# Kernel optimization log

Hardware: AMD Instinct MI355X
Metric: run time of the kernel (lower is better)

Reference implementation:

```python
import jax, jax.numpy as jnp
import numpy as np

N_NODES = 50000
N_EDGES = 800000
N_GRAPHS = 500
DIM = 64          # node feature dim
NG = 64           # num gaussians (edge rbf dim)
CUTOFF = 12.0
NCONV = 3
HID = 128
NTYPES = 100      # atom vocabulary for embedding
EPS = 1e-5        # batchnorm eps


def _bn(x, g, b):
    # training-mode batchnorm over the leading (edge/node) axis
    m = jnp.mean(x, axis=0)
    v = jnp.var(x, axis=0)
    return g * (x - m) * jax.lax.rsqrt(v + EPS) + b


def setup_inputs() -> dict:
    key = jax.random.key(0)
    ks = jax.random.split(key, 12)
    atom_types = jax.random.randint(ks[0], (N_NODES,), 0, NTYPES)
    src = jax.random.randint(ks[1], (N_EDGES,), 0, N_NODES)
    dst = jax.random.randint(ks[2], (N_EDGES,), 0, N_NODES)
    graph_ids = jnp.sort(jax.random.randint(ks[3], (N_NODES,), 0, N_GRAPHS))
    distance = jax.random.uniform(ks[4], (N_EDGES,), dtype=jnp.float32) * CUTOFF
    cin = 2 * DIM + NG
    s = 0.05
    embed_table = jax.random.normal(ks[5], (NTYPES, DIM), dtype=jnp.float32) * s
    W1 = jax.random.normal(ks[6], (NCONV, cin, DIM), dtype=jnp.float32) * s
    b1 = jnp.zeros((NCONV, DIM), jnp.float32)
    W2 = jax.random.normal(ks[7], (NCONV, cin, DIM), dtype=jnp.float32) * s
    b2 = jnp.zeros((NCONV, DIM), jnp.float32)
    g1 = jnp.ones((NCONV, DIM), jnp.float32); bt1 = jnp.zeros((NCONV, DIM), jnp.float32)
    g2 = jnp.ones((NCONV, DIM), jnp.float32); bt2 = jnp.zeros((NCONV, DIM), jnp.float32)
    g3 = jnp.ones((NCONV, DIM), jnp.float32); bt3 = jnp.zeros((NCONV, DIM), jnp.float32)
    Wfc = jax.random.normal(ks[8], (DIM, HID), dtype=jnp.float32) * s
    bfc = jnp.zeros((HID,), jnp.float32)
    Wout = jax.random.normal(ks[9], (HID, 1), dtype=jnp.float32) * s
    bout = jnp.zeros((1,), jnp.float32)
    return dict(atom_types=atom_types, src=src, dst=dst, graph_ids=graph_ids,
                distance=distance, embed_table=embed_table,
                W1=W1, b1=b1, W2=W2, b2=b2,
                g1=g1, bt1=bt1, g2=g2, bt2=bt2, g3=g3, bt3=bt3,
                Wfc=Wfc, bfc=bfc, Wout=Wout, bout=bout)


def reference(atom_types, src, dst, graph_ids, distance, embed_table,
              W1, b1, W2, b2, g1, bt1, g2, bt2, g3, bt3,
              Wfc, bfc, Wout, bout):
    # embedding lookup
    node = embed_table[atom_types]                           # [N, DIM]
    # RBF expansion of distances (gaussian smearing on [0, CUTOFF])
    mu = jnp.linspace(0.0, CUTOFF, NG, dtype=jnp.float32)
    coeff = -0.5 / (mu[1] - mu[0]) ** 2
    rbf = jnp.exp(coeff * (distance[:, None] - mu) ** 2)      # [E, NG]

    for i in range(NCONV):
        # gather: concat(src feats, dst feats, edge rbf)
        te = jnp.concatenate([node[src], node[dst], rbf], axis=-1)  # [E, 192]
        nbr_filter = jax.nn.sigmoid(_bn(te @ W1[i] + b1[i], g1[i], bt1[i]))
        # NOTE: faithful to the source bug: bn2 is applied to nbr_filter,
        # so fc_full2 (W2/b2) output is computed in torch but unused.
        nbr_core = jax.nn.softplus(_bn(nbr_filter, g2[i], bt2[i]))
        h = nbr_filter * nbr_core                              # [E, DIM]
        # scatter-sum messages to destination nodes
        agg = jax.ops.segment_sum(h, dst, num_segments=N_NODES)
        node = node + _bn(agg, g3[i], bt3[i])

    # avg pooling per graph
    sums = jax.ops.segment_sum(node, graph_ids, num_segments=N_GRAPHS)
    cnts = jax.ops.segment_sum(jnp.ones((N_NODES, 1), node.dtype), graph_ids,
                               num_segments=N_GRAPHS)
    crys = sums / jnp.maximum(cnts, 1.0)                       # [G, DIM]

    crys = jax.nn.softplus(crys) @ Wfc + bfc
    crys = jax.nn.softplus(crys)
    return crys @ Wout + bout                                  # [G, 1]
```

## Files before the change

### kernel.cpp

```cpp
#include <hip/hip_runtime.h>
#include <hip/hip_fp16.h>
#include <math.h>

#define DIM 64
#define NG 64
#define CIN 192
#define HID 128
#define NCONV 3
#define TB 8192
#define CUTOFF 12.0f
#define EPS 1e-5f
#define SCB 256

typedef int i2v __attribute__((ext_vector_type(2)));
typedef int i4v __attribute__((ext_vector_type(4)));

__device__ __forceinline__ float sp_(float y) {
    return fmaxf(y, 0.f) + __logf(1.f + __expf(-fabsf(y)));
}
__device__ __forceinline__ float sig_(float y) {
    return 1.f / (1.f + __expf(-y));
}
__device__ __forceinline__ float2 h2f2_bits(int bits) {
    __half2 h;
    __builtin_memcpy(&h, &bits, 4);
    return __half22float2(h);
}
__device__ __forceinline__ int f2h2_bits(float a, float b) {
    __half2 h;
    h.x = __float2half(a);
    h.y = __float2half(b);
    int r;
    __builtin_memcpy(&r, &h, 4);
    return r;
}

__global__ void k_tables(const float* __restrict__ W1, __half2* __restrict__ Tp) {
    int row = blockIdx.x;
    int l = row / TB, i = row % TB;
    int d = threadIdx.x;
    const float stepmu = CUTOFF / (float)(NG - 1);
    const float coeff = -0.5f / (stepmu * stepmu);
    const float stepx = CUTOFF / (float)(TB - 1);
    float x0 = (float)i * stepx;
    float x1 = fminf((float)(i + 1), (float)(TB - 1)) * stepx;
    __shared__ float r0[NG];
    __shared__ float r1[NG];
    float mu = (float)d * stepmu;
    float d0 = x0 - mu, d1 = x1 - mu;
    r0[d] = expf(coeff * d0 * d0);
    r1[d] = expf(coeff * d1 * d1);
    __syncthreads();
    const float* w = W1 + (size_t)(l * CIN + 2 * DIM) * DIM;
    float a0 = 0.f, a1 = 0.f;
#pragma unroll 8
    for (int g = 0; g < NG; ++g) {
        float wv = w[g * DIM + d];
        a0 += r0[g] * wv;
        a1 += r1[g] * wv;
    }
    __half2 hh;
    hh.x = __float2half(a0);
    hh.y = __float2half(a1);
    Tp[(size_t)row * DIM + d] = hh;
}

__global__ void k_hist(const int* __restrict__ dst, int* __restrict__ cnt, int E) {
    for (int e = blockIdx.x * blockDim.x + threadIdx.x; e < E;
         e += gridDim.x * blockDim.x)
        atomicAdd(&cnt[dst[e]], 1);
}

__global__ void k_scanA(const int* __restrict__ cnt, int* __restrict__ bsum, int N) {
    __shared__ int lds[SCB];
    int i = blockIdx.x * SCB + threadIdx.x;
    lds[threadIdx.x] = (i < N) ? cnt[i] : 0;
    __syncthreads();
    for (int o = SCB / 2; o > 0; o >>= 1) {
        if (threadIdx.x < o) lds[threadIdx.x] += lds[threadIdx.x + o];
        __syncthreads();
    }
    if (threadIdx.x == 0) bsum[blockIdx.x] = lds[0];
}

__global__ void k_scanB(const int* __restrict__ bsum, int* __restrict__ bexcl, int NB) {
    __shared__ int lds[SCB];
    int t = threadIdx.x;
    int v = (t < NB) ? bsum[t] : 0;
    lds[t] = v;
    __syncthreads();
    for (int o = 1; o < SCB; o <<= 1) {
        int add = (t >= o) ? lds[t - o] : 0;
        __syncthreads();
        lds[t] += add;
        __syncthreads();
    }
    if (t < NB) bexcl[t] = lds[t] - v;
}

__global__ void k_scanC(const int* __restrict__ cnt, const int* __restrict__ bexcl,
                        int* __restrict__ off, int* __restrict__ cursor, int N, int E) {
    __shared__ int lds[SCB];
    int t = threadIdx.x;
    int i = blockIdx.x * SCB + t;
    int v = (i < N) ? cnt[i] : 0;
    lds[t] = v;
    __syncthreads();
    for (int o = 1; o < SCB; o <<= 1) {
        int add = (t >= o) ? lds[t - o] : 0;
        __syncthreads();
        lds[t] += add;
        __syncthreads();
    }
    if (i < N) {
        int excl = bexcl[blockIdx.x] + lds[t] - v;
        off[i] = excl;
        cursor[i] = excl;
        if (i == N - 1) off[N] = E;
    }
}

__global__ void k_scatter(const int* __restrict__ src, const int* __restrict__ dst,
                          const float* __restrict__ dist, int* __restrict__ cursor,
                          int2* __restrict__ es, int E) {
    const float inv_step = (float)(TB - 1) / CUTOFF;
    for (int e = blockIdx.x * blockDim.x + threadIdx.x; e < E;
         e += gridDim.x * blockDim.x) {
        int t = dst[e];
        int pos = atomicAdd(&cursor[t], 1);
        es[pos] = make_int2(src[e], __float_as_int(dist[e] * inv_step));
    }
}

template <int FIRST>
__global__ void __launch_bounds__(256) k_pq(
        const int* __restrict__ at, const float* __restrict__ emb,
        float* __restrict__ node, const float* __restrict__ agg,
        const double* __restrict__ st, const float* __restrict__ g3,
        const float* __restrict__ bt3, double invN,
        const float* __restrict__ W1, const float* __restrict__ b1, int l,
        __half* __restrict__ P16, float* __restrict__ Q, int N) {
    __shared__ float wa[DIM * DIM];
    __shared__ float wb[DIM * DIM];
    const float* WA = W1 + (size_t)(l * CIN) * DIM;
    for (int k = threadIdx.x; k < DIM * DIM; k += blockDim.x) {
        wa[k] = WA[k];
        wb[k] = WA[DIM * DIM + k];
    }
    int lane = threadIdx.x & 63, w = threadIdx.x >> 6;
    float bv = b1[lane];
    float a3 = 0.f, c3 = 0.f;
    if (!FIRST) {
        double m = st[lane] * invN;
        double v = st[64 + lane] * invN - m * m;
        a3 = g3[lane] / sqrtf((float)v + EPS);
        c3 = bt3[lane] - a3 * (float)m;
    }
    __syncthreads();
    int wpb = blockDim.x >> 6;
    for (int n = blockIdx.x * wpb + w; n < N; n += gridDim.x * wpb) {
        float nv;
        if (FIRST) {
            nv = emb[at[n] * DIM + lane];
        } else {
            nv = node[n * DIM + lane] + a3 * agg[n * DIM + lane] + c3;
        }
        node[n * DIM + lane] = nv;
        float ap = 0.f, aq = bv;
#pragma unroll 8
        for (int k = 0; k < DIM; ++k) {
            float b = __shfl(nv, k);
            ap += b * wa[k * DIM + lane];
            aq += b * wb[k * DIM + lane];
        }
        P16[n * DIM + lane] = __float2half(ap);
        Q[n * DIM + lane] = aq;
    }
}

__global__ void __launch_bounds__(256) k_convA(
        const int* __restrict__ off, const int2* __restrict__ es,
        const __half* __restrict__ P16, const float* __restrict__ Q,
        const __half2* __restrict__ Tp,
        double* __restrict__ stats, __half* __restrict__ z16, int N) {
    int lane = threadIdx.x & 63;
    int w = threadIdx.x >> 6;
    int dg = lane & 15;
    int slot = lane >> 4;
    int d0 = dg * 4;
    float s00 = 0.f, s01 = 0.f, s02 = 0.f, s03 = 0.f;
    float s10 = 0.f, s11 = 0.f, s12 = 0.f, s13 = 0.f;
    int gw = blockIdx.x * 4 + w, nw = gridDim.x * 4;
    for (int n = gw; n < N; n += nw) {
        int e0 = off[n], e1 = off[n + 1];
        if (e0 >= e1) continue;
        float4 q4 = *(const float4*)(Q + (size_t)n * DIM + d0);
        for (int eb = e0; eb < e1; eb += 4) {
            int e = eb + slot;
            bool valid = (e < e1);
            int ec = valid ? e : (e1 - 1);
            int2 ev = es[ec];
            float u = __int_as_float(ev.y);
            int i = (int)u;
            i = max(0, min(i, TB - 2));
            float fr = u - (float)i;
            i2v pb = *(const i2v*)(P16 + (size_t)ev.x * DIM + d0);
            i4v tb = *(const i4v*)(Tp + (size_t)i * DIM + d0);
            float2 p01 = h2f2_bits(pb.x), p23 = h2f2_bits(pb.y);
            float2 t0 = h2f2_bits(tb.x), t1 = h2f2_bits(tb.y);
            float2 t2 = h2f2_bits(tb.z), t3 = h2f2_bits(tb.w);
            float z0 = p01.x + t0.x + fr * (t0.y - t0.x) + q4.x;
            float z1 = p01.y + t1.x + fr * (t1.y - t1.x) + q4.y;
            float z2 = p23.x + t2.x + fr * (t2.y - t2.x) + q4.z;
            float z3 = p23.y + t3.x + fr * (t3.y - t3.x) + q4.w;
            if (valid) {
                i2v zz;
                zz.x = f2h2_bits(z0, z1);
                zz.y = f2h2_bits(z2, z3);
                *(i2v*)(z16 + (size_t)e * DIM + d0) = zz;
                s00 += z0; s10 += z0 * z0;
                s01 += z1; s11 += z1 * z1;
                s02 += z2; s12 += z2 * z2;
                s03 += z3; s13 += z3 * z3;
            }
        }
    }
    __shared__ float r0[4][64][4];
    __shared__ float r1[4][64][4];
    r0[w][lane][0] = s00; r0[w][lane][1] = s01;
    r0[w][lane][2] = s02; r0[w][lane][3] = s03;
    r1[w][lane][0] = s10; r1[w][lane][1] = s11;
    r1[w][lane][2] = s12; r1[w][lane][3] = s13;
    __syncthreads();
    if (threadIdx.x < 64) {
        int d = threadIdx.x;
        int dgg = d >> 2, q = d & 3;
        float t0 = 0.f, t1 = 0.f;
#pragma unroll
        for (int ww = 0; ww < 4; ++ww)
#pragma unroll
            for (int sl = 0; sl < 4; ++sl) {
                t0 += r0[ww][sl * 16 + dgg][q];
                t1 += r1[ww][sl * 16 + dgg][q];
            }
        atomicAdd(&stats[d], (double)t0);
        atomicAdd(&stats[64 + d], (double)t1);
    }
}

__global__ void __launch_bounds__(256) k_statsF(
        __half* __restrict__ zf16,
        const double* __restrict__ stA, const float* __restrict__ gA,
        const float* __restrict__ btA,
        double* __restrict__ stats, int total8, double invE) {
    int gq = threadIdx.x & 7;
    float a1[8], c1[8];
#pragma unroll
    for (int q = 0; q < 8; ++q) {
        int d = gq * 8 + q;
        double m = stA[d] * invE;
        double v = stA[64 + d] * invE - m * m;
        a1[q] = gA[d] / sqrtf((float)v + EPS);
        c1[q] = btA[d] - a1[q] * (float)m;
    }
    float s0[8] = {0, 0, 0, 0, 0, 0, 0, 0};
    float s1[8] = {0, 0, 0, 0, 0, 0, 0, 0};
    i4v* z4 = (i4v*)zf16;
    int tid = blockIdx.x * blockDim.x + threadIdx.x;
    int stride = gridDim.x * blockDim.x;
    for (int i = tid; i < total8; i += stride) {
        i4v v = z4[i];
        float2 p0 = h2f2_bits(v.x);
        float2 p1 = h2f2_bits(v.y);
        float2 p2 = h2f2_bits(v.z);
        float2 p3 = h2f2_bits(v.w);
        float f0 = sig_(a1[0] * p0.x + c1[0]);
        float f1 = sig_(a1[1] * p0.y + c1[1]);
        float f2 = sig_(a1[2] * p1.x + c1[2]);
        float f3 = sig_(a1[3] * p1.y + c1[3]);
        float f4 = sig_(a1[4] * p2.x + c1[4]);
        float f5 = sig_(a1[5] * p2.y + c1[5]);
        float f6 = sig_(a1[6] * p3.x + c1[6]);
        float f7 = sig_(a1[7] * p3.y + c1[7]);
        i4v o;
        o.x = f2h2_bits(f0, f1);
        o.y = f2h2_bits(f2, f3);
        o.z = f2h2_bits(f4, f5);
        o.w = f2h2_bits(f6, f7);
        z4[i] = o;
        s0[0] += f0; s1[0] += f0 * f0;
        s0[1] += f1; s1[1] += f1 * f1;
        s0[2] += f2; s1[2] += f2 * f2;
        s0[3] += f3; s1[3] += f3 * f3;
        s0[4] += f4; s1[4] += f4 * f4;
        s0[5] += f5; s1[5] += f5 * f5;
        s0[6] += f6; s1[6] += f6 * f6;
        s0[7] += f7; s1[7] += f7 * f7;
    }
    __shared__ float lds[256][16];
#pragma unroll
    for (int q = 0; q < 8; ++q) {
        lds[threadIdx.x][q] = s0[q];
        lds[threadIdx.x][8 + q] = s1[q];
    }
    __syncthreads();
    if (threadIdx.x < 64) {
        int d = threadIdx.x;
        int grp = d >> 3, j = d & 7;
        float t0 = 0.f, t1 = 0.f;
        for (int k = 0; k < 32; ++k) {
            int t = k * 8 + grp;
            t0 += lds[t][j];
            t1 += lds[t][8 + j];
        }
        atomicAdd(&stats[d], (double)t0);
        atomicAdd(&stats[64 + d], (double)t1);
    }
}

__global__ void __launch_bounds__(256) k_aggF(
        const int* __restrict__ off, const __half* __restrict__ f16,
        const double* __restrict__ stB, const float* __restrict__ gB,
        const float* __restrict__ btB,
        double* __restrict__ stats, float* __restrict__ agg, int N, double invE) {
    int lane = threadIdx.x & 63;
    int w = threadIdx.x >> 6;
    int dg = lane & 7;
    int slot = lane >> 3;
    int d0 = dg * 8;
    float a2[8], c2[8];
#pragma unroll
    for (int q = 0; q < 8; ++q) {
        int d = d0 + q;
        double m = stB[d] * invE, v = stB[64 + d] * invE - m * m;
        a2[q] = gB[d] / sqrtf((float)v + EPS);
        c2[q] = btB[d] - a2[q] * (float)m;
    }
    float s0[8] = {0, 0, 0, 0, 0, 0, 0, 0};
    float s1[8] = {0, 0, 0, 0, 0, 0, 0, 0};
    int gw = blockIdx.x * 4 + w, nw = gridDim.x * 4;
    for (int n = gw; n < N; n += nw) {
        int e0 = off[n], e1 = off[n + 1];
        float tot[8] = {0, 0, 0, 0, 0, 0, 0, 0};
        for (int eb = e0; eb < e1; eb += 8) {
            int e = eb + slot;
            float mk = (e < e1) ? 1.f : 0.f;
            int ec = (e < e1) ? e : (e1 - 1);
            i4v zb = *(const i4v*)(f16 + (size_t)ec * DIM + d0);
            float2 zp0 = h2f2_bits(zb.x);
            float2 zp1 = h2f2_bits(zb.y);
            float2 zp2 = h2f2_bits(zb.z);
            float2 zp3 = h2f2_bits(zb.w);
            float fv[8] = {zp0.x, zp0.y, zp1.x, zp1.y, zp2.x, zp2.y, zp3.x, zp3.y};
#pragma unroll
            for (int q = 0; q < 8; ++q) {
                float h = fv[q] * sp_(a2[q] * fv[q] + c2[q]);
                tot[q] += mk * h;
            }
        }
#pragma unroll
        for (int q = 0; q < 8; ++q) {
            float v = tot[q];
            v += __shfl_xor(v, 8);
            v += __shfl_xor(v, 16);
            v += __shfl_xor(v, 32);
            tot[q] = v;
        }
        if (slot == 0) {
            float4 w0 = make_float4(tot[0], tot[1], tot[2], tot[3]);
            float4 w1 = make_float4(tot[4], tot[5], tot[6], tot[7]);
            *(float4*)(agg + (size_t)n * DIM + d0) = w0;
            *(float4*)(agg + (size_t)n * DIM + d0 + 4) = w1;
#pragma unroll
            for (int q = 0; q < 8; ++q) {
                s0[q] += tot[q];
                s1[q] += tot[q] * tot[q];
            }
        }
    }
    __shared__ float r0[4][8][8];
    __shared__ float r1[4][8][8];
    if (slot == 0) {
#pragma unroll
        for (int q = 0; q < 8; ++q) {
            r0[w][dg][q] = s0[q];
            r1[w][dg][q] = s1[q];
        }
    }
    __syncthreads();
    if (threadIdx.x < 64) {
        int d = threadIdx.x;
        int dgg = d >> 3, q = d & 7;
        float t0 = 0.f, t1 = 0.f;
#pragma unroll
        for (int ww = 0; ww < 4; ++ww) {
            t0 += r0[ww][dgg][q];
            t1 += r1[ww][dgg][q];
        }
        atomicAdd(&stats[d], (double)t0);
        atomicAdd(&stats[64 + d], (double)t1);
    }
}

template <int MODE>
__global__ void __launch_bounds__(256) k_conv(
        const int* __restrict__ off, const int2* __restrict__ es,
        const __half* __restrict__ P16, const float* __restrict__ Q,
        const __half2* __restrict__ Tp,
        const double* __restrict__ stA, const float* __restrict__ gA,
        const float* __restrict__ btA,
        const double* __restrict__ stB, const float* __restrict__ gB,
        const float* __restrict__ btB,
        double* __restrict__ stats, float* __restrict__ agg, int N, double invE) {
    int lane = threadIdx.x & 63;
    int w = threadIdx.x >> 6;
    float a1 = 0.f, c1 = 0.f, a2 = 0.f, c2 = 0.f;
    if (MODE >= 2) {
        double m = stA[lane] * invE;
        double v = stA[64 + lane] * invE - m * m;
        a1 = gA[lane] / sqrtf((float)v + EPS);
        c1 = btA[lane] - a1 * (float)m;
    }
    if (MODE == 3) {
        double m = stB[lane] * invE;
        double v = stB[64 + lane] * invE - m * m;
        a2 = gB[lane] / sqrtf((float)v + EPS);
        c2 = btB[lane] - a2 * (float)m;
    }
    float s0 = 0.f, s1 = 0.f;
    int gw = blockIdx.x * 4 + w, nw = gridDim.x * 4;
    for (int n = gw; n < N; n += nw) {
        int e0 = off[n], e1 = off[n + 1];
        float qc = Q[n * DIM + lane];
        float acc = 0.f;
        auto body = [&](int2 ev) {
            float u = __int_as_float(ev.y);
            int i = (int)u;
            i = max(0, min(i, TB - 2));
            float fr = u - (float)i;
            float2 t2 = __half22float2(Tp[(size_t)i * DIM + lane]);
            float p = __half2float(P16[(size_t)ev.x * DIM + lane]);
            float z = p + t2.x + fr * (t2.y - t2.x) + qc;
            if (MODE == 0) { s0 += z; s1 += z * z; }
            else {
                float f = sig_(a1 * z + c1);
                if (MODE == 2) { s0 += f; s1 += f * f; }
                else acc += f * sp_(a2 * f + c2);
            }
        };
        int e = e0;
        for (; e + 2 <= e1; e += 2) { body(es[e]); body(es[e + 1]); }
        if (e < e1) body(es[e]);
        if (MODE == 3) {
            agg[n * DIM + lane] = acc;
            s0 += acc; s1 += acc * acc;
        }
    }
    __shared__ float r0[4][64];
    __shared__ float r1[4][64];
    r0[w][lane] = s0;
    r1[w][lane] = s1;
    __syncthreads();
    if (threadIdx.x < 64) {
        int d = threadIdx.x;
        float t0 = r0[0][d] + r0[1][d] + r0[2][d] + r0[3][d];
        float t1 = r1[0][d] + r1[1][d] + r1[2][d] + r1[3][d];
        atomicAdd(&stats[d], (double)t0);
        atomicAdd(&stats[64 + d], (double)t1);
    }
}

__global__ void k_head(const float* __restrict__ node, const float* __restrict__ agg,
                       const double* __restrict__ st, const float* __restrict__ g3,
                       const float* __restrict__ bt3, double invN,
                       const int* __restrict__ gid, int N,
                       const float* __restrict__ Wfc, const float* __restrict__ bfc,
                       const float* __restrict__ Wout, const float* __restrict__ bout,
                       float* __restrict__ out) {
    int g = blockIdx.x;
    __shared__ int bounds[2];
    if (threadIdx.x == 0) {
        int lo = 0, hi = N;
        while (lo < hi) { int mid = (lo + hi) >> 1; if (gid[mid] < g) lo = mid + 1; else hi = mid; }
        bounds[0] = lo;
        int lo2 = lo; hi = N;
        while (lo2 < hi) { int mid = (lo2 + hi) >> 1; if (gid[mid] < g + 1) lo2 = mid + 1; else hi = mid; }
        bounds[1] = lo2;
    }
    __syncthreads();
    int s = bounds[0], e = bounds[1];
    __shared__ float sp[DIM];
    if (threadIdx.x < DIM) {
        int d = threadIdx.x;
        double mm = st[d] * invN;
        double vv = st[64 + d] * invN - mm * mm;
        float a3 = g3[d] / sqrtf((float)vv + EPS);
        float c3 = bt3[d] - a3 * (float)mm;
        float sn = 0.f, sa = 0.f;
        for (int n = s; n < e; ++n) {
            sn += node[(size_t)n * DIM + d];
            sa += agg[(size_t)n * DIM + d];
        }
        float cntf = (float)max(e - s, 1);
        float m = (sn + a3 * sa) / cntf + c3;
        sp[d] = (m > 0.f) ? m + log1pf(expf(-m)) : log1pf(expf(m));
    }
    __syncthreads();
    int j = threadIdx.x;
    float hj = bfc[j];
#pragma unroll 8
    for (int k = 0; k < DIM; ++k) hj += sp[k] * Wfc[k * HID + j];
    hj = (hj > 0.f) ? hj + log1pf(expf(-hj)) : log1pf(expf(hj));
    __shared__ float red[HID];
    red[j] = hj * Wout[j];
    __syncthreads();
    for (int o = HID / 2; o > 0; o >>= 1) {
        if (j < o) red[j] += red[j + o];
        __syncthreads();
    }
    if (j == 0) out[g] = red[0] + bout[0];
}

extern "C" void kernel_launch(void* const* d_in, const int* in_sizes, int n_in,
                              void* d_out, int out_size, void* d_ws, size_t ws_size,
                              hipStream_t stream) {
    const int* atom_types = (const int*)d_in[0];
    const int* src = (const int*)d_in[1];
    const int* dst = (const int*)d_in[2];
    const int* gid = (const int*)d_in[3];
    const float* dist = (const float*)d_in[4];
    const float* emb = (const float*)d_in[5];
    const float* W1 = (const float*)d_in[6];
    const float* b1 = (const float*)d_in[7];
    const float* g1 = (const float*)d_in[10];
    const float* bt1 = (const float*)d_in[11];
    const float* g2 = (const float*)d_in[12];
    const float* bt2 = (const float*)d_in[13];
    const float* g3 = (const float*)d_in[14];
    const float* bt3 = (const float*)d_in[15];
    const float* Wfc = (const float*)d_in[16];
    const float* bfc = (const float*)d_in[17];
    const float* Wout = (const float*)d_in[18];
    const float* bout = (const float*)d_in[19];

    int N = in_sizes[0];
    int E = in_sizes[1];
    int G = out_size;
    int NB = (N + SCB - 1) / SCB;

    char* ws = (char*)d_ws;
    auto alloc = [&](size_t bytes) -> char* {
        char* p = ws;
        ws += (bytes + 255) & ~(size_t)255;
        return p;
    };
    size_t nd = (size_t)N * DIM * sizeof(float);
    float* node = (float*)alloc(nd);
    __half* P16 = (__half*)alloc(nd / 2);
    float* Q = (float*)alloc(nd);
    float* agg = (float*)alloc(nd);
    __half2* Tp = (__half2*)alloc((size_t)NCONV * TB * DIM * sizeof(__half2));
    double* stats = (double*)alloc((size_t)NCONV * 3 * 128 * sizeof(double));
    int* off = (int*)alloc((size_t)(N + 1) * sizeof(int));
    int* cursor = (int*)alloc((size_t)N * sizeof(int));
    int* cnt = (int*)alloc((size_t)N * sizeof(int));
    int* bsum = (int*)alloc(SCB * sizeof(int));
    int* bexcl = (int*)alloc(SCB * sizeof(int));
    int2* es = (int2*)alloc((size_t)E * sizeof(int2));
    size_t zbytes = (size_t)E * DIM * sizeof(__half);
    size_t used = (size_t)(ws - (char*)d_ws);
    bool planZ = (used + zbytes) <= ws_size;
    __half* z16 = planZ ? (__half*)alloc(zbytes) : nullptr;

    hipMemsetAsync(stats, 0, (size_t)NCONV * 3 * 128 * sizeof(double), stream);
    hipMemsetAsync(cnt, 0, (size_t)N * sizeof(int), stream);

    k_tables<<<NCONV * TB, 64, 0, stream>>>(W1, Tp);

    k_hist<<<1024, 256, 0, stream>>>(dst, cnt, E);
    k_scanA<<<NB, SCB, 0, stream>>>(cnt, bsum, N);
    k_scanB<<<1, SCB, 0, stream>>>(bsum, bexcl, NB);
    k_scanC<<<NB, SCB, 0, stream>>>(cnt, bexcl, off, cursor, N, E);
    k_scatter<<<1024, 256, 0, stream>>>(src, dst, dist, cursor, es, E);

    double invE = 1.0 / (double)E;
    double invN = 1.0 / (double)N;

    for (int l = 0; l < NCONV; ++l) {
        const __half2* Tl = Tp + (size_t)l * TB * DIM;
        double* st1 = stats + (size_t)(l * 3 + 0) * 128;
        double* st2 = stats + (size_t)(l * 3 + 1) * 128;
        double* st3 = stats + (size_t)(l * 3 + 2) * 128;

        if (l == 0) {
            k_pq<1><<<2048, 256, 0, stream>>>(atom_types, emb, node, nullptr,
                                              nullptr, nullptr, nullptr, 0.0,
                                              W1, b1 + l * DIM, l, P16, Q, N);
        } else {
            double* st3p = stats + (size_t)((l - 1) * 3 + 2) * 128;
            k_pq<0><<<2048, 256, 0, stream>>>(atom_types, emb, node, agg,
                                              st3p, g3 + (l - 1) * DIM,
                                              bt3 + (l - 1) * DIM, invN,
                                              W1, b1 + l * DIM, l, P16, Q, N);
        }

        if (planZ) {
            k_convA<<<2048, 256, 0, stream>>>(off, es, P16, Q, Tl, st1, z16, N);
            k_statsF<<<2048, 256, 0, stream>>>(z16, st1, g1 + l * DIM, bt1 + l * DIM,
                                               st2, E * 8, invE);
            k_aggF<<<2048, 256, 0, stream>>>(off, z16,
                                             st2, g2 + l * DIM, bt2 + l * DIM,
                                             st3, agg, N, invE);
        } else {
            k_conv<0><<<2048, 256, 0, stream>>>(off, es, P16, Q, Tl,
                                                nullptr, nullptr, nullptr,
                                                nullptr, nullptr, nullptr,
                                                st1, nullptr, N, invE);
            k_conv<2><<<2048, 256, 0, stream>>>(off, es, P16, Q, Tl,
                                                st1, g1 + l * DIM, bt1 + l * DIM,
                                                nullptr, nullptr, nullptr,
                                                st2, nullptr, N, invE);
            k_conv<3><<<2048, 256, 0, stream>>>(off, es, P16, Q, Tl,
                                                st1, g1 + l * DIM, bt1 + l * DIM,
                                                st2, g2 + l * DIM, bt2 + l * DIM,
                                                st3, agg, N, invE);
        }
    }

    double* st3f = stats + (size_t)(2 * 3 + 2) * 128;
    k_head<<<G, HID, 0, stream>>>(node, agg, st3f, g3 + 2 * DIM, bt3 + 2 * DIM,
                                  invN, gid, N, Wfc, bfc, Wout, bout, (float*)d_out);
}
```

Before: 983.3 us.

## Unroll per-node edge loops by two and shrink RBF interpolation table

The edge loops in the convolution gather kernel and the aggregation kernel now handle two edges per lane per iteration. Their independent gathers can be issued together, giving more memory-level parallelism on the latency-bound loads. The precomputed RBF/weight interpolation table is reduced from 8192 to 2048 entries so it fits better in cache. The cost is coarser linear interpolation of the Gaussian filter contribution, which slightly reduces accuracy, plus more wasted masked work on low-degree nodes.

```diff
diff --git a/kernel.cpp b/kernel.cpp
--- a/kernel.cpp
+++ b/kernel.cpp
@@ -7,7 +7,7 @@
 #define CIN 192
 #define HID 128
 #define NCONV 3
-#define TB 8192
+#define TB 2048
 #define CUTOFF 12.0f
 #define EPS 1e-5f
 #define SCB 256
@@ -195,33 +195,57 @@
         int e0 = off[n], e1 = off[n + 1];
         if (e0 >= e1) continue;
         float4 q4 = *(const float4*)(Q + (size_t)n * DIM + d0);
-        for (int eb = e0; eb < e1; eb += 4) {
-            int e = eb + slot;
-            bool valid = (e < e1);
-            int ec = valid ? e : (e1 - 1);
-            int2 ev = es[ec];
-            float u = __int_as_float(ev.y);
-            int i = (int)u;
-            i = max(0, min(i, TB - 2));
-            float fr = u - (float)i;
-            i2v pb = *(const i2v*)(P16 + (size_t)ev.x * DIM + d0);
-            i4v tb = *(const i4v*)(Tp + (size_t)i * DIM + d0);
-            float2 p01 = h2f2_bits(pb.x), p23 = h2f2_bits(pb.y);
-            float2 t0 = h2f2_bits(tb.x), t1 = h2f2_bits(tb.y);
-            float2 t2 = h2f2_bits(tb.z), t3 = h2f2_bits(tb.w);
-            float z0 = p01.x + t0.x + fr * (t0.y - t0.x) + q4.x;
-            float z1 = p01.y + t1.x + fr * (t1.y - t1.x) + q4.y;
-            float z2 = p23.x + t2.x + fr * (t2.y - t2.x) + q4.z;
-            float z3 = p23.y + t3.x + fr * (t3.y - t3.x) + q4.w;
-            if (valid) {
-                i2v zz;
-                zz.x = f2h2_bits(z0, z1);
-                zz.y = f2h2_bits(z2, z3);
-                *(i2v*)(z16 + (size_t)e * DIM + d0) = zz;
-                s00 += z0; s10 += z0 * z0;
-                s01 += z1; s11 += z1 * z1;
-                s02 += z2; s12 += z2 * z2;
-                s03 += z3; s13 += z3 * z3;
+        for (int eb = e0; eb < e1; eb += 8) {
+            int eA = eb + slot, eB = eA + 4;
+            bool vA = (eA < e1), vB = (eB < e1);
+            int2 evA = es[vA ? eA : e1 - 1];
+            int2 evB = es[vB ? eB : e1 - 1];
+            float uA = __int_as_float(evA.y), uB = __int_as_float(evB.y);
+            int iA = (int)uA, iB = (int)uB;
+            iA = max(0, min(iA, TB - 2));
+            iB = max(0, min(iB, TB - 2));
+            float frA = uA - (float)iA, frB = uB - (float)iB;
+            i2v pbA = *(const i2v*)(P16 + (size_t)evA.x * DIM + d0);
+            i2v pbB = *(const i2v*)(P16 + (size_t)evB.x * DIM + d0);
+            i4v tbA = *(const i4v*)(Tp + (size_t)iA * DIM + d0);
+            i4v tbB = *(const i4v*)(Tp + (size_t)iB * DIM + d0);
+            {
+                float2 p01 = h2f2_bits(pbA.x), p23 = h2f2_bits(pbA.y);
+                float2 t0 = h2f2_bits(tbA.x), t1 = h2f2_bits(tbA.y);
+                float2 t2 = h2f2_bits(tbA.z), t3 = h2f2_bits(tbA.w);
+                float z0 = p01.x + t0.x + frA * (t0.y - t0.x) + q4.x;
+                float z1 = p01.y + t1.x + frA * (t1.y - t1.x) + q4.y;
+                float z2 = p23.x + t2.x + frA * (t2.y - t2.x) + q4.z;
+                float z3 = p23.y + t3.x + frA * (t3.y - t3.x) + q4.w;
+                if (vA) {
+                    i2v zz;
+                    zz.x = f2h2_bits(z0, z1);
+                    zz.y = f2h2_bits(z2, z3);
+                    *(i2v*)(z16 + (size_t)eA * DIM + d0) = zz;
+                    s00 += z0; s10 += z0 * z0;
+                    s01 += z1; s11 += z1 * z1;
+                    s02 += z2; s12 += z2 * z2;
+                    s03 += z3; s13 += z3 * z3;
+                }
+            }
+            {
+                float2 p01 = h2f2_bits(pbB.x), p23 = h2f2_bits(pbB.y);
+                float2 t0 = h2f2_bits(tbB.x), t1 = h2f2_bits(tbB.y);
+                float2 t2 = h2f2_bits(tbB.z), t3 = h2f2_bits(tbB.w);
+                float z0 = p01.x + t0.x + frB * (t0.y - t0.x) + q4.x;
+                float z1 = p01.y + t1.x + frB * (t1.y - t1.x) + q4.y;
+                float z2 = p23.x + t2.x + frB * (t2.y - t2.x) + q4.z;
+                float z3 = p23.y + t3.x + frB * (t3.y - t3.x) + q4.w;
+                if (vB) {
+                    i2v zz;
+                    zz.x = f2h2_bits(z0, z1);
+                    zz.y = f2h2_bits(z2, z3);
+                    *(i2v*)(z16 + (size_t)eB * DIM + d0) = zz;
+                    s00 += z0; s10 += z0 * z0;
+                    s01 += z1; s11 += z1 * z1;
+                    s02 += z2; s12 += z2 * z2;
+                    s03 += z3; s13 += z3 * z3;
+                }
             }
         }
     }
@@ -342,20 +366,25 @@
     for (int n = gw; n < N; n += nw) {
         int e0 = off[n], e1 = off[n + 1];
         float tot[8] = {0, 0, 0, 0, 0, 0, 0, 0};
-        for (int eb = e0; eb < e1; eb += 8) {
-            int e = eb + slot;
-            float mk = (e < e1) ? 1.f : 0.f;
-            int ec = (e < e1) ? e : (e1 - 1);
-            i4v zb = *(const i4v*)(f16 + (size_t)ec * DIM + d0);
-            float2 zp0 = h2f2_bits(zb.x);
-            float2 zp1 = h2f2_bits(zb.y);
-            float2 zp2 = h2f2_bits(zb.z);
-            float2 zp3 = h2f2_bits(zb.w);
-            float fv[8] = {zp0.x, zp0.y, zp1.x, zp1.y, zp2.x, zp2.y, zp3.x, zp3.y};
+        for (int eb = e0; eb < e1; eb += 16) {
+            int eA = eb + slot, eB = eA + 8;
+            float mkA = (eA < e1) ? 1.f : 0.f;
+            float mkB = (eB < e1) ? 1.f : 0.f;
+            int ecA = (eA < e1) ? eA : (e1 - 1);
+            int ecB = (eB < e1) ? eB : (e1 - 1);
+            i4v zbA = *(const i4v*)(f16 + (size_t)ecA * DIM + d0);
+            i4v zbB = *(const i4v*)(f16 + (size_t)ecB * DIM + d0);
+            float2 a0 = h2f2_bits(zbA.x), a1v = h2f2_bits(zbA.y);
+            float2 a2v = h2f2_bits(zbA.z), a3v = h2f2_bits(zbA.w);
+            float2 b0 = h2f2_bits(zbB.x), b1v = h2f2_bits(zbB.y);
+            float2 b2v = h2f2_bits(zbB.z), b3v = h2f2_bits(zbB.w);
+            float fA[8] = {a0.x, a0.y, a1v.x, a1v.y, a2v.x, a2v.y, a3v.x, a3v.y};
+            float fB[8] = {b0.x, b0.y, b1v.x, b1v.y, b2v.x, b2v.y, b3v.x, b3v.y};
 #pragma unroll
             for (int q = 0; q < 8; ++q) {
-                float h = fv[q] * sp_(a2[q] * fv[q] + c2[q]);
-                tot[q] += mk * h;
+                float hA = fA[q] * sp_(a2[q] * fA[q] + c2[q]);
+                float hB = fB[q] * sp_(a2[q] * fB[q] + c2[q]);
+                tot[q] += mkA * hA + mkB * hB;
             }
         }
 #pragma unroll
```

New measurement: 971.8 us. About the same (-1.2%).
